# Kernel optimization log

Hardware: AMD Instinct MI355X
Metric: run time of the kernel (lower is better)

The kernel has to match this reference:

```python
import jax, jax.numpy as jnp
import numpy as np

MEM_LEN = 2048      # memory_len
N_TURNS = 8         # user-facing n_turns (module stores N_TURNS+1)
RATE = 2            # compression_rate
B, S, D = 32, 512, 1024
N_CONV = sum(RATE ** i for i in range(1, N_TURNS + 1))  # 510


def setup_inputs() -> dict:
    key = jax.random.key(0)
    k1, k2, k3 = jax.random.split(key, 3)
    inputs = jax.random.normal(k1, (B, S, D), dtype=jnp.float32)
    memory = jax.random.normal(k2, (MEM_LEN + N_CONV, D), dtype=jnp.float32)
    filters = jax.random.normal(k3, (RATE, D, D), dtype=jnp.float32) * (1.0 / np.sqrt(RATE * D))
    return {"inputs": inputs, "memory": memory, "filters": filters}


def _compress(x, filters):
    # x: (L, D) -> (L // RATE, D): strided VALID conv1d, filter (width=RATE, in=D, out=D)
    y = jax.lax.conv_general_dilated(
        x[None], filters, window_strides=(RATE,), padding='VALID',
        dimension_numbers=('NWC', 'WIO', 'NWC'))
    return y[0]


def _memory_pass(x, memory, filters):
    # x: (S, D); replicates HelixMemory._memory_pass for one batch element.
    new_memory = jnp.concatenate([memory, x], axis=0)        # (MEM_LEN+N_CONV+S, D)
    short = new_memory[-MEM_LEN:]                            # (MEM_LEN, D)
    long_mem = new_memory[:-MEM_LEN][:-S]                    # (N_CONV, D)
    fallout = short[-S:]                                     # (S, D) == x (S<=MEM_LEN)
    helix = jnp.concatenate([long_mem, _compress(fallout, filters)], axis=0)  # (N_CONV+S//RATE, D)
    new_mem = short
    # stored n_turns = N_TURNS+1; loop k = 1..N_TURNS (unrolled, all shapes static)
    for k in range(1, N_TURNS + 1):
        n_long = sum(RATE ** i for i in range(1, N_TURNS + 2 - k))
        turn = RATE ** (N_TURNS + 1 - k)
        add = helix.shape[0] - n_long                         # > 0 for all k here
        old = helix[-turn - add:-add]                         # (turn, D)
        part = helix[-turn:]                                  # (turn, D)
        helix = jnp.concatenate([helix[:-turn - add], _compress(old, filters)], axis=0)
        new_mem = jnp.concatenate([part, new_mem], axis=0)
    return new_mem                                            # (MEM_LEN+N_CONV, D)


def reference(inputs, memory, filters):
    # (B, S, D) -> (B, MEM_LEN+N_CONV, D)
    return jax.vmap(lambda x: _memory_pass(x, memory, filters))(inputs)
```

## Files before the change

kernel.cpp:

```cpp
#include <hip/hip_runtime.h>
#include <hip/hip_bf16.h>

#define B_SZ 32
#define S_SZ 512
#define D_SZ 1024
#define OUT_ROW_STRIDE 2558
#define K_DIM 2048
#define M_BATCH 8192
#define M_TOTAL 8448
#define N_DIM 1024

typedef _Float16 half8 __attribute__((ext_vector_type(8)));
typedef _Float16 half4v __attribute__((ext_vector_type(4)));
typedef float f32x4 __attribute__((ext_vector_type(4)));

__device__ __forceinline__ void async_copy16(const void* g, void* l) {
    __builtin_amdgcn_global_load_lds(
        (const __attribute__((address_space(1))) unsigned int*)g,
        (__attribute__((address_space(3))) unsigned int*)l, 16, 0, 0);
}

__global__ __launch_bounds__(256) void transpose_w(const float* __restrict__ f,
                                                   _Float16* __restrict__ wt) {
    __shared__ float tile[32][33];
    const int k0 = blockIdx.x * 32;
    const int n0 = blockIdx.y * 32;
    const int tx = threadIdx.x;
    const int ty = threadIdx.y;
#pragma unroll
    for (int i = 0; i < 32; i += 8)
        tile[ty + i][tx] = f[(size_t)(k0 + ty + i) * 1024 + n0 + tx];
    __syncthreads();
#pragma unroll
    for (int i = 0; i < 32; i += 8)
        wt[(size_t)(n0 + ty + i) * 2048 + k0 + tx] = (_Float16)tile[tx][ty + i];
}

__global__ __launch_bounds__(256) void convert_a(const float* __restrict__ inputs,
                                                 const float* __restrict__ memory,
                                                 _Float16* __restrict__ a16) {
    const int m = blockIdx.x;
    const int c = threadIdx.x * 8;
    const float* src = nullptr;
    if (m < M_BATCH) {
        src = inputs + (size_t)m * 2048;
    } else {
        int r = m - M_BATCH;
        if (r < 254) src = memory + (size_t)(2 * r + 2) * 1024;
    }
    half8 h;
    if (src) {
        float4 v0 = *(const float4*)(src + c);
        float4 v1 = *(const float4*)(src + c + 4);
        h[0] = (_Float16)v0.x; h[1] = (_Float16)v0.y;
        h[2] = (_Float16)v0.z; h[3] = (_Float16)v0.w;
        h[4] = (_Float16)v1.x; h[5] = (_Float16)v1.y;
        h[6] = (_Float16)v1.z; h[7] = (_Float16)v1.w;
    } else {
#pragma unroll
        for (int i = 0; i < 8; ++i) h[i] = (_Float16)0.f;
    }
    *(half8*)(a16 + (size_t)m * 2048 + c) = h;
}

__global__ __launch_bounds__(256) void gemm_async(const _Float16* __restrict__ a16,
                                                  const _Float16* __restrict__ wt,
                                                  float* __restrict__ out,
                                                  float* __restrict__ ws_c) {
    __shared__ _Float16 a_lds[128 * 32];
    __shared__ _Float16 b_lds[128 * 32];

    const int tid = threadIdx.x;
    const int m_base = blockIdx.x * 128;
    const int n_base = blockIdx.y * 128;

    const int wave = tid >> 6;
    const int lane = tid & 63;
    const int q = lane >> 4;
    const int lm = lane & 15;
    const int wm = (wave >> 1) * 64;
    const int wn = (wave & 1) * 64;

    const int srow = wave * 16 + (lane >> 2);
    const int kc = (lane & 3) * 8;
    const _Float16* ag0 = a16 + (size_t)(m_base + srow) * 2048 + kc;
    const _Float16* ag1 = a16 + (size_t)(m_base + 64 + srow) * 2048 + kc;
    const _Float16* bg0 = wt + (size_t)(n_base + srow) * 2048 + kc;
    const _Float16* bg1 = wt + (size_t)(n_base + 64 + srow) * 2048 + kc;
    _Float16* al0 = a_lds + wave * 512;
    _Float16* al1 = a_lds + 2048 + wave * 512;
    _Float16* bl0 = b_lds + wave * 512;
    _Float16* bl1 = b_lds + 2048 + wave * 512;

    f32x4 acc[4][4] = {};

    for (int kt = 0; kt < K_DIM / 32; ++kt) {
        const int k0 = kt * 32;
        __syncthreads();
        async_copy16(ag0 + k0, al0);
        async_copy16(ag1 + k0, al1);
        async_copy16(bg0 + k0, bl0);
        async_copy16(bg1 + k0, bl1);
        __syncthreads();

        half8 a_frag[4], b_frag[4];
#pragma unroll
        for (int t = 0; t < 4; ++t) {
            a_frag[t] = *(const half8*)(&a_lds[(wm + t * 16 + lm) * 32 + q * 8]);
            b_frag[t] = *(const half8*)(&b_lds[(wn + t * 16 + lm) * 32 + q * 8]);
        }
#pragma unroll
        for (int i = 0; i < 4; ++i)
#pragma unroll
            for (int j = 0; j < 4; ++j)
                acc[i][j] = __builtin_amdgcn_mfma_f32_16x16x32_f16(a_frag[i], b_frag[j],
                                                                   acc[i][j], 0, 0, 0);
    }

#pragma unroll
    for (int i = 0; i < 4; ++i) {
        const int m0 = m_base + wm + i * 16 + q * 4;
#pragma unroll
        for (int j = 0; j < 4; ++j) {
            const int n = n_base + wn + j * 16 + lm;
#pragma unroll
            for (int rg = 0; rg < 4; ++rg) {
                const int m = m0 + rg;
                const float v = acc[i][j][rg];
                if (m < M_BATCH) {
                    const int b = m >> 8;
                    const int row = 254 + (m & 255);
                    out[(size_t)b * (OUT_ROW_STRIDE * D_SZ) + (size_t)row * 1024 + n] = v;
                } else {
                    const int r = m - M_BATCH;
                    if (r < 254) ws_c[(size_t)r * 1024 + n] = v;
                }
            }
        }
    }
}

#define LDS_STRIDE 40
__global__ __launch_bounds__(256) void gemm_fallback(const float* __restrict__ inputs,
                                                     const float* __restrict__ memory,
                                                     const _Float16* __restrict__ wt,
                                                     float* __restrict__ out,
                                                     float* __restrict__ ws_c) {
    __shared__ _Float16 a_lds[128 * LDS_STRIDE];
    __shared__ _Float16 b_lds[128 * LDS_STRIDE];
    const int tid = threadIdx.x;
    const int m_base = blockIdx.x * 128;
    const int n_base = blockIdx.y * 128;
    const int wave = tid >> 6, lane = tid & 63;
    const int q = lane >> 4, lm = lane & 15;
    const int wm = (wave >> 1) * 64, wn = (wave & 1) * 64;
    f32x4 acc[4][4] = {};
    const float* a_src[4];
#pragma unroll
    for (int it = 0; it < 4; ++it) {
        int pos = it * 256 + tid;
        int row = pos >> 3;
        int m = m_base + row;
        const float* p = nullptr;
        if (m < M_BATCH) p = inputs + (size_t)m * 2048;
        else { int r = m - M_BATCH; if (r < 254) p = memory + (size_t)(2 * r + 2) * 1024; }
        a_src[it] = p;
    }
    for (int kt = 0; kt < K_DIM / 32; ++kt) {
        const int k0 = kt * 32;
        __syncthreads();
#pragma unroll
        for (int it = 0; it < 4; ++it) {
            int pos = it * 256 + tid;
            int row = pos >> 3, c4 = pos & 7;
            float4 v = {0.f, 0.f, 0.f, 0.f};
            if (a_src[it]) v = *(const float4*)(a_src[it] + k0 + c4 * 4);
            half4v h;
            h[0] = (_Float16)v.x; h[1] = (_Float16)v.y;
            h[2] = (_Float16)v.z; h[3] = (_Float16)v.w;
            *(half4v*)(&a_lds[row * LDS_STRIDE + c4 * 4]) = h;
        }
#pragma unroll
        for (int it = 0; it < 2; ++it) {
            int pos = it * 256 + tid;
            int row = pos >> 2, c8 = pos & 3;
            uint4 v = *(const uint4*)(wt + (size_t)(n_base + row) * 2048 + k0 + c8 * 8);
            *(uint4*)(&b_lds[row * LDS_STRIDE + c8 * 8]) = v;
        }
        __syncthreads();
        half8 a_frag[4], b_frag[4];
#pragma unroll
        for (int t = 0; t < 4; ++t) {
            a_frag[t] = *(const half8*)(&a_lds[(wm + t * 16 + lm) * LDS_STRIDE + q * 8]);
            b_frag[t] = *(const half8*)(&b_lds[(wn + t * 16 + lm) * LDS_STRIDE + q * 8]);
        }
#pragma unroll
        for (int i = 0; i < 4; ++i)
#pragma unroll
            for (int j = 0; j < 4; ++j)
                acc[i][j] = __builtin_amdgcn_mfma_f32_16x16x32_f16(a_frag[i], b_frag[j],
                                                                   acc[i][j], 0, 0, 0);
    }
#pragma unroll
    for (int i = 0; i < 4; ++i) {
        const int m0 = m_base + wm + i * 16 + q * 4;
#pragma unroll
        for (int j = 0; j < 4; ++j) {
            const int n = n_base + wn + j * 16 + lm;
#pragma unroll
            for (int rg = 0; rg < 4; ++rg) {
                const int m = m0 + rg;
                const float v = acc[i][j][rg];
                if (m < M_BATCH) {
                    const int b = m >> 8;
                    const int row = 254 + (m & 255);
                    out[(size_t)b * (OUT_ROW_STRIDE * D_SZ) + (size_t)row * 1024 + n] = v;
                } else {
                    const int r = m - M_BATCH;
                    if (r < 254) ws_c[(size_t)r * 1024 + n] = v;
                }
            }
        }
    }
}

__global__ __launch_bounds__(256) void assemble_kernel(const float* __restrict__ inputs,
                                                       const float* __restrict__ memory,
                                                       const float* __restrict__ ws_c,
                                                       float* __restrict__ out) {
    const int b = blockIdx.y;
    const int r = blockIdx.x;
    const int col = threadIdx.x * 4;
    float4 v;
    size_t dst_row;
    if (r < 254) {
        v = *(const float4*)(ws_c + (size_t)r * 1024 + col);
        dst_row = r;
    } else if (r < 1790) {
        v = *(const float4*)(memory + (size_t)(1022 + r - 254) * 1024 + col);
        dst_row = 510 + (r - 254);
    } else {
        v = *(const float4*)(inputs + (size_t)b * (S_SZ * D_SZ) + (size_t)(r - 1790) * 1024 + col);
        dst_row = 2046 + (r - 1790);
    }
    *(float4*)(out + (size_t)b * (OUT_ROW_STRIDE * D_SZ) + dst_row * 1024 + col) = v;
}

extern "C" void kernel_launch(void* const* d_in, const int* in_sizes, int n_in,
                              void* d_out, int out_size, void* d_ws, size_t ws_size,
                              hipStream_t stream) {
    const float* inputs  = (const float*)d_in[0];
    const float* memory  = (const float*)d_in[1];
    const float* filters = (const float*)d_in[2];
    float* out = (float*)d_out;

    const size_t WT_BYTES  = (size_t)N_DIM * K_DIM * 2;
    const size_t A16_BYTES = (size_t)M_TOTAL * K_DIM * 2;
    const size_t NEED = WT_BYTES + A16_BYTES + (size_t)254 * 1024 * 4;

    _Float16* wt = (_Float16*)d_ws;
    transpose_w<<<dim3(64, 32), dim3(32, 8), 0, stream>>>(filters, wt);

    if (ws_size >= NEED) {
        _Float16* a16 = (_Float16*)((char*)d_ws + WT_BYTES);
        float* ws_c   = (float*)((char*)d_ws + WT_BYTES + A16_BYTES);
        convert_a<<<dim3(M_TOTAL), 256, 0, stream>>>(inputs, memory, a16);
        gemm_async<<<dim3(66, 8), 256, 0, stream>>>(a16, wt, out, ws_c);
        assemble_kernel<<<dim3(2302, 32), 256, 0, stream>>>(inputs, memory, ws_c, out);
    } else {
        float* ws_c = (float*)((char*)d_ws + WT_BYTES);
        gemm_fallback<<<dim3(66, 8), 256, 0, stream>>>(inputs, memory, wt, out, ws_c);
        assemble_kernel<<<dim3(2302, 32), 256, 0, stream>>>(inputs, memory, ws_c, out);
    }
}
```

Before: 519.2 us.

## Retile GEMM to 128x64 with K=64 swizzled LDS, fuse input copy into conversion

The GEMM tile changes from 128x128 with K-step 32 to 128x64 with K-step 64. The LDS layout is XOR-swizzled to avoid bank conflicts, the grid doubles in N, and launch bounds hint at 4 blocks per CU for occupancy. The convert kernel now also writes the raw input rows into the output tail while it has them loaded, so the assemble kernel no longer re-reads inputs and handles only the compressed and memory rows. In exchange, the narrower N tile re-reads the A operand more often.

```diff
diff --git a/kernel.cpp b/kernel.cpp
--- a/kernel.cpp
+++ b/kernel.cpp
@@ -38,12 +38,16 @@
 
 __global__ __launch_bounds__(256) void convert_a(const float* __restrict__ inputs,
                                                  const float* __restrict__ memory,
-                                                 _Float16* __restrict__ a16) {
+                                                 _Float16* __restrict__ a16,
+                                                 float* __restrict__ out) {
     const int m = blockIdx.x;
-    const int c = threadIdx.x * 8;
+    const int t = threadIdx.x;
+    const int c = t * 8;
     const float* src = nullptr;
+    bool is_batch = false;
     if (m < M_BATCH) {
         src = inputs + (size_t)m * 2048;
+        is_batch = true;
     } else {
         int r = m - M_BATCH;
         if (r < 254) src = memory + (size_t)(2 * r + 2) * 1024;
@@ -56,6 +60,16 @@
         h[2] = (_Float16)v0.z; h[3] = (_Float16)v0.w;
         h[4] = (_Float16)v1.x; h[5] = (_Float16)v1.y;
         h[6] = (_Float16)v1.z; h[7] = (_Float16)v1.w;
+        if (is_batch) {
+            const int b = m >> 8;
+            const int w = m & 255;
+            const int hi = t >> 7;
+            const int col = (t & 127) * 8;
+            float* dst = out + (size_t)b * (OUT_ROW_STRIDE * D_SZ)
+                             + (size_t)(2046 + 2 * w + hi) * 1024 + col;
+            *(float4*)dst = v0;
+            *(float4*)(dst + 4) = v1;
+        }
     } else {
 #pragma unroll
         for (int i = 0; i < 8; ++i) h[i] = (_Float16)0.f;
@@ -63,70 +77,87 @@
     *(half8*)(a16 + (size_t)m * 2048 + c) = h;
 }
 
-__global__ __launch_bounds__(256) void gemm_async(const _Float16* __restrict__ a16,
-                                                  const _Float16* __restrict__ wt,
-                                                  float* __restrict__ out,
-                                                  float* __restrict__ ws_c) {
-    __shared__ _Float16 a_lds[128 * 32];
-    __shared__ _Float16 b_lds[128 * 32];
+__global__ __launch_bounds__(256, 4) void gemm_async(const _Float16* __restrict__ a16,
+                                                     const _Float16* __restrict__ wt,
+                                                     float* __restrict__ out,
+                                                     float* __restrict__ ws_c) {
+    __shared__ _Float16 a_lds[128 * 64];
+    __shared__ _Float16 b_lds[64 * 64];
 
     const int tid = threadIdx.x;
     const int m_base = blockIdx.x * 128;
-    const int n_base = blockIdx.y * 128;
+    const int n_base = blockIdx.y * 64;
 
     const int wave = tid >> 6;
     const int lane = tid & 63;
     const int q = lane >> 4;
     const int lm = lane & 15;
     const int wm = (wave >> 1) * 64;
-    const int wn = (wave & 1) * 64;
-
-    const int srow = wave * 16 + (lane >> 2);
-    const int kc = (lane & 3) * 8;
-    const _Float16* ag0 = a16 + (size_t)(m_base + srow) * 2048 + kc;
-    const _Float16* ag1 = a16 + (size_t)(m_base + 64 + srow) * 2048 + kc;
-    const _Float16* bg0 = wt + (size_t)(n_base + srow) * 2048 + kc;
-    const _Float16* bg1 = wt + (size_t)(n_base + 64 + srow) * 2048 + kc;
-    _Float16* al0 = a_lds + wave * 512;
-    _Float16* al1 = a_lds + 2048 + wave * 512;
-    _Float16* bl0 = b_lds + wave * 512;
-    _Float16* bl1 = b_lds + 2048 + wave * 512;
-
-    f32x4 acc[4][4] = {};
-
-    for (int kt = 0; kt < K_DIM / 32; ++kt) {
-        const int k0 = kt * 32;
+    const int wn = (wave & 1) * 32;
+
+    const int srow = lane >> 3;
+    const int g = (lane & 7) ^ srow;
+    const int koff = g * 8;
+
+    const _Float16* ag[4];
+    _Float16* al[4];
+#pragma unroll
+    for (int i = 0; i < 4; ++i) {
+        int row = wave * 32 + i * 8 + srow;
+        ag[i] = a16 + (size_t)(m_base + row) * 2048 + koff;
+        al[i] = a_lds + (wave * 32 + i * 8) * 64;
+    }
+    const _Float16* bg[2];
+    _Float16* bl[2];
+#pragma unroll
+    for (int i = 0; i < 2; ++i) {
+        int row = wave * 16 + i * 8 + srow;
+        bg[i] = wt + (size_t)(n_base + row) * 2048 + koff;
+        bl[i] = b_lds + (wave * 16 + i * 8) * 64;
+    }
+
+    f32x4 acc[4][2] = {};
+
+    const int sw = lm & 7;
+
+    for (int kt = 0; kt < K_DIM / 64; ++kt) {
+        const int k0 = kt * 64;
         __syncthreads();
-        async_copy16(ag0 + k0, al0);
-        async_copy16(ag1 + k0, al1);
-        async_copy16(bg0 + k0, bl0);
-        async_copy16(bg1 + k0, bl1);
+#pragma unroll
+        for (int i = 0; i < 4; ++i) async_copy16(ag[i] + k0, al[i]);
+#pragma unroll
+        for (int i = 0; i < 2; ++i) async_copy16(bg[i] + k0, bl[i]);
         __syncthreads();
 
-        half8 a_frag[4], b_frag[4];
-#pragma unroll
-        for (int t = 0; t < 4; ++t) {
-            a_frag[t] = *(const half8*)(&a_lds[(wm + t * 16 + lm) * 32 + q * 8]);
-            b_frag[t] = *(const half8*)(&b_lds[(wn + t * 16 + lm) * 32 + q * 8]);
-        }
-#pragma unroll
-        for (int i = 0; i < 4; ++i)
-#pragma unroll
-            for (int j = 0; j < 4; ++j)
-                acc[i][j] = __builtin_amdgcn_mfma_f32_16x16x32_f16(a_frag[i], b_frag[j],
-                                                                   acc[i][j], 0, 0, 0);
-    }
-
-#pragma unroll
-    for (int i = 0; i < 4; ++i) {
-        const int m0 = m_base + wm + i * 16 + q * 4;
-#pragma unroll
-        for (int j = 0; j < 4; ++j) {
-            const int n = n_base + wn + j * 16 + lm;
+#pragma unroll
+        for (int h = 0; h < 2; ++h) {
+            const int phys = ((h * 4 + q) ^ sw) * 8;
+            half8 a_frag[4], b_frag[2];
+#pragma unroll
+            for (int t = 0; t < 4; ++t)
+                a_frag[t] = *(const half8*)(&a_lds[(wm + t * 16 + lm) * 64 + phys]);
+#pragma unroll
+            for (int u = 0; u < 2; ++u)
+                b_frag[u] = *(const half8*)(&b_lds[(wn + u * 16 + lm) * 64 + phys]);
+#pragma unroll
+            for (int t = 0; t < 4; ++t)
+#pragma unroll
+                for (int u = 0; u < 2; ++u)
+                    acc[t][u] = __builtin_amdgcn_mfma_f32_16x16x32_f16(
+                        a_frag[t], b_frag[u], acc[t][u], 0, 0, 0);
+        }
+    }
+
+#pragma unroll
+    for (int t = 0; t < 4; ++t) {
+        const int m0 = m_base + wm + t * 16 + q * 4;
+#pragma unroll
+        for (int u = 0; u < 2; ++u) {
+            const int n = n_base + wn + u * 16 + lm;
 #pragma unroll
             for (int rg = 0; rg < 4; ++rg) {
                 const int m = m0 + rg;
-                const float v = acc[i][j][rg];
+                const float v = acc[t][u][rg];
                 if (m < M_BATCH) {
                     const int b = m >> 8;
                     const int row = 254 + (m & 255);
@@ -138,6 +169,24 @@
             }
         }
     }
+}
+
+__global__ __launch_bounds__(256) void assemble_small(const float* __restrict__ memory,
+                                                      const float* __restrict__ ws_c,
+                                                      float* __restrict__ out) {
+    const int b = blockIdx.y;
+    const int r = blockIdx.x;
+    const int col = threadIdx.x * 4;
+    float4 v;
+    size_t dst_row;
+    if (r < 254) {
+        v = *(const float4*)(ws_c + (size_t)r * 1024 + col);
+        dst_row = r;
+    } else {
+        v = *(const float4*)(memory + (size_t)(1022 + r - 254) * 1024 + col);
+        dst_row = 510 + (r - 254);
+    }
+    *(float4*)(out + (size_t)b * (OUT_ROW_STRIDE * D_SZ) + dst_row * 1024 + col) = v;
 }
 
 #define LDS_STRIDE 40
@@ -224,10 +273,10 @@
     }
 }
 
-__global__ __launch_bounds__(256) void assemble_kernel(const float* __restrict__ inputs,
-                                                       const float* __restrict__ memory,
-                                                       const float* __restrict__ ws_c,
-                                                       float* __restrict__ out) {
+__global__ __launch_bounds__(256) void assemble_full(const float* __restrict__ inputs,
+                                                     const float* __restrict__ memory,
+                                                     const float* __restrict__ ws_c,
+                                                     float* __restrict__ out) {
     const int b = blockIdx.y;
     const int r = blockIdx.x;
     const int col = threadIdx.x * 4;
@@ -264,12 +313,12 @@
     if (ws_size >= NEED) {
         _Float16* a16 = (_Float16*)((char*)d_ws + WT_BYTES);
         float* ws_c   = (float*)((char*)d_ws + WT_BYTES + A16_BYTES);
-        convert_a<<<dim3(M_TOTAL), 256, 0, stream>>>(inputs, memory, a16);
-        gemm_async<<<dim3(66, 8), 256, 0, stream>>>(a16, wt, out, ws_c);
-        assemble_kernel<<<dim3(2302, 32), 256, 0, stream>>>(inputs, memory, ws_c, out);
+        convert_a<<<dim3(M_TOTAL), 256, 0, stream>>>(inputs, memory, a16, out);
+        gemm_async<<<dim3(66, 16), 256, 0, stream>>>(a16, wt, out, ws_c);
+        assemble_small<<<dim3(1790, 32), 256, 0, stream>>>(memory, ws_c, out);
     } else {
         float* ws_c = (float*)((char*)d_ws + WT_BYTES);
         gemm_fallback<<<dim3(66, 8), 256, 0, stream>>>(inputs, memory, wt, out, ws_c);
-        assemble_kernel<<<dim3(2302, 32), 256, 0, stream>>>(inputs, memory, ws_c, out);
-    }
-}
+        assemble_full<<<dim3(2302, 32), 256, 0, stream>>>(inputs, memory, ws_c, out);
+    }
+}
```

After: 482.4 us. 7.1% less time.
